# Performance work log

Measured on AMD Instinct MI355X. Metric: run time of the kernel, lower is better.

## Reference

```python
import jax, jax.numpy as jnp
import numpy as np

B, L, D_SINGLE, D_PAIR = 1, 768, 384, 128


def setup_inputs() -> dict:
    key = jax.random.key(0)
    k_s, k_z, k_w, k_b = jax.random.split(key, 4)
    s = jax.random.normal(k_s, (B, L, D_SINGLE), dtype=jnp.float32)
    z = jax.random.normal(k_z, (B, L, L, D_PAIR), dtype=jnp.float32)
    # nn.Linear(2*d_single, d_pair): weight [d_pair, 2*d_single], bias [d_pair]
    bound = 1.0 / np.sqrt(2 * D_SINGLE)
    W = jax.random.uniform(k_w, (2 * D_SINGLE, D_PAIR), dtype=jnp.float32,
                           minval=-bound, maxval=bound)
    bias = jax.random.uniform(k_b, (D_PAIR,), dtype=jnp.float32,
                              minval=-bound, maxval=bound)
    return {"s": s, "z": z, "W": W, "bias": bias}


def reference(s, z, W, bias):
    # proj(cat([a, b], -1)) decomposes: W = [W1; W2] along input dim.
    # out[b,i,j] = s[b,i] @ W1 + s[b,j] @ W2 + bias  (never materialize z_cat)
    D = s.shape[-1]
    W1, W2 = W[:D], W[D:]
    left = jnp.einsum('bld,df->blf', s, W1)   # [B, L, d_pair]
    right = jnp.einsum('bld,df->blf', s, W2)  # [B, L, d_pair]
    out = left[:, :, None, :] + right[:, None, :, :] + bias  # [B, L, L, d_pair]
    return out
```

## Files before the change

### kernel.cpp

```cpp
#include <hip/hip_runtime.h>
#include <hip/hip_bf16.h>


#define L_DIM   768
#define D_S     384
#define D_P     128

__global__ __launch_bounds__(256) void proj_kernel(
    const float* __restrict__ s,
    const float* __restrict__ W,
    const float* __restrict__ bias,
    float* __restrict__ proj)
{
    __shared__ float s_row[D_S];
    const int l = blockIdx.x;
    const int f = threadIdx.x;

    for (int d = threadIdx.x; d < D_S; d += 256) s_row[d] = s[l * D_S + d];
    __syncthreads();

    const int fc = f & (D_P - 1);
    const float* Wbase = W + ((f >= D_P) ? (D_S * D_P) : 0) + fc;

    float acc = (f < D_P) ? bias[fc] : 0.0f;
#pragma unroll 8
    for (int d = 0; d < D_S; ++d) {
        acc = fmaf(s_row[d], Wbase[(size_t)d * D_P], acc);
    }
    proj[l * 256 + f] = acc;
}

__global__ __launch_bounds__(256) void outer_kernel(
    const float4* __restrict__ proj4,
    float4* __restrict__ out4)
{
    const int i  = blockIdx.y;
    const int t  = blockIdx.x * 256 + threadIdx.x;
    const int f4 = t & 31;
    const int j  = t >> 5;

    const float4 lv = proj4[i * 64 + f4];
    const float4 rv = proj4[j * 64 + 32 + f4];

    float4 o;
    o.x = lv.x + rv.x;
    o.y = lv.y + rv.y;
    o.z = lv.z + rv.z;
    o.w = lv.w + rv.w;

    out4[(size_t)i * (L_DIM * (D_P / 4)) + t] = o;
}

extern "C" void kernel_launch(void* const* d_in, const int* in_sizes, int n_in,
                              void* d_out, int out_size, void* d_ws, size_t ws_size,
                              hipStream_t stream) {
    const float* s    = (const float*)d_in[0];
    const float* W    = (const float*)d_in[2];
    const float* bias = (const float*)d_in[3];
    float* out  = (float*)d_out;
    float* proj = (float*)d_ws;

    proj_kernel<<<dim3(L_DIM), dim3(256), 0, stream>>>(s, W, bias, proj);

    outer_kernel<<<dim3(L_DIM * (D_P / 4) / 256, L_DIM), dim3(256), 0, stream>>>(
        (const float4*)proj, (float4*)out);
}
```

Before: 440.7 us.

## Vectorize projection, batch rows per block, use nontemporal stores in outer kernel

The projection kernel now handles four rows per block with float4 weight loads, so each thread computes four outputs and fewer blocks re-read W. The outer kernel has each thread write four j positions, reusing the left vector and issuing nontemporal stores for the large output. The aim is to cut the cost of write-bandwidth-bound output streaming and the redundant weight traffic. Nontemporal stores bypass cache retention, which may or may not help on this hardware.

After: 450.9 us. +2.3%, slower.

```diff
diff --git a/kernel.cpp b/kernel.cpp
--- a/kernel.cpp
+++ b/kernel.cpp
@@ -1,54 +1,74 @@
 #include <hip/hip_runtime.h>
-#include <hip/hip_bf16.h>
 
 
 #define L_DIM   768
 #define D_S     384
 #define D_P     128
 
+typedef float f32x4 __attribute__((ext_vector_type(4)));
+
 __global__ __launch_bounds__(256) void proj_kernel(
-    const float* __restrict__ s,
-    const float* __restrict__ W,
-    const float* __restrict__ bias,
-    float* __restrict__ proj)
+    const float4* __restrict__ s4,
+    const float4* __restrict__ W4,
+    const float4* __restrict__ bias4,
+    float4* __restrict__ proj4)
 {
-    __shared__ float s_row[D_S];
-    const int l = blockIdx.x;
-    const int f = threadIdx.x;
+    __shared__ float s_rows[4][D_S];
+    const int tid = threadIdx.x;
+    const int r   = tid >> 6;
+    const int c   = tid & 63;
+    const int l0  = blockIdx.x * 4;
 
-    for (int d = threadIdx.x; d < D_S; d += 256) s_row[d] = s[l * D_S + d];
+    {
+        const float4* src = s4 + (size_t)l0 * (D_S / 4);
+        float4* dst = (float4*)&s_rows[0][0];
+        for (int idx = tid; idx < 4 * (D_S / 4); idx += 256) dst[idx] = src[idx];
+    }
     __syncthreads();
 
-    const int fc = f & (D_P - 1);
-    const float* Wbase = W + ((f >= D_P) ? (D_S * D_P) : 0) + fc;
+    const int     right = (c >= 32);
+    const int     f4    = c & 31;
+    const float4* Wb    = W4 + (size_t)(right ? D_S : 0) * (D_P / 4) + f4;
+    const float*  srow  = s_rows[r];
 
-    float acc = (f < D_P) ? bias[fc] : 0.0f;
+    float4 acc = right ? make_float4(0.f, 0.f, 0.f, 0.f) : bias4[f4];
+
 #pragma unroll 8
     for (int d = 0; d < D_S; ++d) {
-        acc = fmaf(s_row[d], Wbase[(size_t)d * D_P], acc);
+        const float  sv = srow[d];
+        const float4 w  = Wb[(size_t)d * (D_P / 4)];
+        acc.x = fmaf(sv, w.x, acc.x);
+        acc.y = fmaf(sv, w.y, acc.y);
+        acc.z = fmaf(sv, w.z, acc.z);
+        acc.w = fmaf(sv, w.w, acc.w);
     }
-    proj[l * 256 + f] = acc;
+    proj4[(size_t)(l0 + r) * 64 + c] = acc;
 }
 
+#define JPT 4
 __global__ __launch_bounds__(256) void outer_kernel(
     const float4* __restrict__ proj4,
     float4* __restrict__ out4)
 {
-    const int i  = blockIdx.y;
-    const int t  = blockIdx.x * 256 + threadIdx.x;
-    const int f4 = t & 31;
-    const int j  = t >> 5;
+    const int i   = blockIdx.y;
+    const int tid = threadIdx.x;
+    const int f4  = tid & 31;
+    const int jg  = tid >> 5;
+    const int j0  = blockIdx.x * (8 * JPT) + jg * JPT;
 
-    const float4 lv = proj4[i * 64 + f4];
-    const float4 rv = proj4[j * 64 + 32 + f4];
+    const float4 lv = proj4[(size_t)i * 64 + f4];
+    f32x4* obase = (f32x4*)(out4 + ((size_t)i * L_DIM + j0) * (D_P / 4) + f4);
 
-    float4 o;
-    o.x = lv.x + rv.x;
-    o.y = lv.y + rv.y;
-    o.z = lv.z + rv.z;
-    o.w = lv.w + rv.w;
-
-    out4[(size_t)i * (L_DIM * (D_P / 4)) + t] = o;
+#pragma unroll
+    for (int k = 0; k < JPT; ++k) {
+        const float4 rv = proj4[(size_t)(j0 + k) * 64 + 32 + f4];
+        f32x4 o;
+        o.x = lv.x + rv.x;
+        o.y = lv.y + rv.y;
+        o.z = lv.z + rv.z;
+        o.w = lv.w + rv.w;
+        __builtin_nontemporal_store(o, obase + (size_t)k * (D_P / 4));
+    }
 }
 
 extern "C" void kernel_launch(void* const* d_in, const int* in_sizes, int n_in,
@@ -60,8 +80,9 @@
     float* out  = (float*)d_out;
     float* proj = (float*)d_ws;
 
-    proj_kernel<<<dim3(L_DIM), dim3(256), 0, stream>>>(s, W, bias, proj);
+    proj_kernel<<<dim3(L_DIM / 4), dim3(256), 0, stream>>>(
+        (const float4*)s, (const float4*)W, (const float4*)bias, (float4*)proj);
 
-    outer_kernel<<<dim3(L_DIM * (D_P / 4) / 256, L_DIM), dim3(256), 0, stream>>>(
+    outer_kernel<<<dim3(L_DIM / (8 * JPT), L_DIM), dim3(256), 0, stream>>>(
         (const float4*)proj, (float4*)out);
 }
```
